# Performance work log

Hardware: AMD Instinct MI355X
Metric: run time of the kernel (lower is better)

## Reference

```python
import jax, jax.numpy as jnp
import numpy as np

B, T, D = 64, 2048, 300

def setup_inputs() -> dict:
    key = jax.random.key(0)
    k1, k2, k3, k4 = jax.random.split(key, 4)
    gate_encoding = jax.random.uniform(k1, (B, T, D), dtype=jnp.float32)
    inputs_encoding = jax.random.normal(k2, (B, T, D), dtype=jnp.float32)
    # kaiming-normal-ish init: std = sqrt(2 / fan_in)
    std = float(np.sqrt(2.0 / D))
    Wz = jax.random.normal(k3, (D, D), dtype=jnp.float32) * std
    Wo = jax.random.normal(k4, (D, D), dtype=jnp.float32) * std
    bz = jnp.zeros((D,), dtype=jnp.float32)
    bo = jnp.zeros((D,), dtype=jnp.float32)
    return {"gate_encoding": gate_encoding, "inputs_encoding": inputs_encoding,
            "Wz": Wz, "bz": bz, "Wo": Wo, "bo": bo}

def reference(gate_encoding, inputs_encoding, Wz, bz, Wo, bo):
    # Batch the two linear projections across all timesteps (torch.nn.Linear: x @ W.T + b)
    z = jnp.tanh(jnp.einsum('btd,ed->bte', inputs_encoding, Wz) + bz)  # [B,T,D]
    o = jnp.tanh(jnp.einsum('btd,ed->bte', inputs_encoding, Wo) + bo)  # [B,T,D]

    # Sequential gated recurrence: c_t = g_t * c_{t-1} + (1 - g_t) * z_t ; h_t = o_t * c_t
    def step(c, gz_o):
        g_t, z_t, o_t = gz_o
        c = g_t * c + (1.0 - g_t) * z_t
        return c, o_t * c

    c0 = jnp.zeros((gate_encoding.shape[0], gate_encoding.shape[2]), dtype=inputs_encoding.dtype)
    # scan over time: move T to leading axis
    _, h = jax.lax.scan(step, c0,
                        (jnp.swapaxes(gate_encoding, 0, 1),
                         jnp.swapaxes(z, 0, 1),
                         jnp.swapaxes(o, 0, 1)))
    return jnp.swapaxes(h, 0, 1)  # [B,T,D]
```

## Files before the change

kernel.cpp:

```cpp
#include <hip/hip_runtime.h>
#include <hip/hip_bf16.h>

typedef _Float16 f16x8 __attribute__((ext_vector_type(8)));
typedef _Float16 f16x4 __attribute__((ext_vector_type(4)));
typedef float f32x4 __attribute__((ext_vector_type(4)));

#define B_SZ 64
#define T_SZ 2048
#define D_SZ 300
#define M_SZ (B_SZ * T_SZ)
#define KP 320
#define NP 640
#define NCHUNK 32
#define CLEN 64

__device__ __forceinline__ void gld_lds16(const void* g, void* l) {
    __builtin_amdgcn_global_load_lds(
        (const __attribute__((address_space(1))) unsigned int*)g,
        (__attribute__((address_space(3))) unsigned int*)l,
        16, 0, 0);
}

__device__ __forceinline__ float fast_tanh(float x) {
    float e = __expf(2.0f * x);
    return 1.0f - 2.0f * __builtin_amdgcn_rcpf(e + 1.0f);
}

__global__ void pack_x(const float* __restrict__ in, _Float16* __restrict__ out) {
    unsigned int i = blockIdx.x * 256u + threadIdx.x;
    f32x4 v = *(const f32x4*)(in + (size_t)i * 4);
#pragma unroll
    for (int j = 0; j < 4; ++j) {
        unsigned int f = i * 4 + j;
        unsigned int row = f / D_SZ;
        unsigned int k = f - row * D_SZ;
        out[(size_t)row * KP + k] = (_Float16)v[j];
    }
}

__global__ void pad_x(_Float16* __restrict__ out) {
    unsigned int i = blockIdx.x * 256u + threadIdx.x;
    unsigned int j = i * 4;
    unsigned int row = j / 20;
    unsigned int k0 = j - row * 20;
    f16x4 z = {};
    *(f16x4*)(out + (size_t)row * KP + 300 + k0) = z;
}

__global__ void pack_w(const float* __restrict__ Wz, const float* __restrict__ Wo,
                       _Float16* __restrict__ W) {
    unsigned int i = blockIdx.x * 256u + threadIdx.x;
    if (i >= NP * KP) return;
    unsigned int n = i / KP;
    unsigned int k = i - n * KP;
    float v = 0.0f;
    if (k < D_SZ) {
        if (n < D_SZ) v = Wz[n * D_SZ + k];
        else if (n >= 320 && n < 320 + D_SZ) v = Wo[(n - 320) * D_SZ + k];
    }
    W[i] = (_Float16)v;
}

__global__ void pack_bias(const float* __restrict__ bz, const float* __restrict__ bo,
                          float* __restrict__ bias) {
    int n = threadIdx.x;
    float v = 0.0f;
    if (n < D_SZ) v = bz[n];
    else if (n >= 320 && n < 320 + D_SZ) v = bo[n - 320];
    bias[n] = v;
}

__global__ __launch_bounds__(256) void gemm_zo(const _Float16* __restrict__ X,
                                               const _Float16* __restrict__ W,
                                               const float* __restrict__ bias,
                                               _Float16* __restrict__ C) {
    __shared__ _Float16 As[3][128 * 32];
    __shared__ _Float16 Bs[3][128 * 32];

    const int tid = threadIdx.x;
    const int lane = tid & 63;
    const int wid = tid >> 6;
    const int wm = wid >> 1, wn = wid & 1;

    int g = blockIdx.x;
    int s = (g & 7) * (5120 / 8) + (g >> 3);
    int bm = s / 5;
    int bn = s - bm * 5;

    f32x4 acc[4][4] = {};

    const int r_in_c = lane >> 2;
    const int u_phys = lane & 3;

    const _Float16* Abase = X + (size_t)(bm * 128) * KP;
    const _Float16* Bbase = W + (size_t)(bn * 128) * KP;

    auto stage = [&](int buf, int kt) {
#pragma unroll
        for (int j = 0; j < 2; ++j) {
            int c = wid + j * 4;
            int row = c * 16 + r_in_c;
            int ul = u_phys ^ ((row >> 1) & 3);
            gld_lds16(Abase + (size_t)row * KP + kt * 32 + ul * 8, &As[buf][c * 512]);
            gld_lds16(Bbase + (size_t)row * KP + kt * 32 + ul * 8, &Bs[buf][c * 512]);
        }
    };

    stage(0, 0);
    stage(1, 1);

#pragma unroll 1
    for (int kt = 0; kt < 10; ++kt) {
        if (kt < 8) {
            stage((kt + 2) % 3, kt + 2);
            asm volatile("s_waitcnt vmcnt(8)" ::: "memory");
        } else if (kt == 8) {
            asm volatile("s_waitcnt vmcnt(4)" ::: "memory");
        } else {
            asm volatile("s_waitcnt vmcnt(0)" ::: "memory");
        }
        __builtin_amdgcn_s_barrier();
        __builtin_amdgcn_sched_barrier(0);

        const int cb = kt % 3;
        f16x8 bf[4], af[4];
#pragma unroll
        for (int ns = 0; ns < 4; ++ns) {
            int row = wn * 64 + ns * 16 + (lane & 15);
            int u = (lane >> 4) ^ ((row >> 1) & 3);
            bf[ns] = *(const f16x8*)&Bs[cb][row * 32 + u * 8];
        }
#pragma unroll
        for (int ms = 0; ms < 4; ++ms) {
            int row = wm * 64 + ms * 16 + (lane & 15);
            int u = (lane >> 4) ^ ((row >> 1) & 3);
            af[ms] = *(const f16x8*)&As[cb][row * 32 + u * 8];
        }
        asm volatile("s_waitcnt lgkmcnt(0)" ::: "memory");
        __builtin_amdgcn_s_barrier();
        __builtin_amdgcn_sched_barrier(0);

        __builtin_amdgcn_s_setprio(1);
#pragma unroll
        for (int ms = 0; ms < 4; ++ms)
#pragma unroll
            for (int ns = 0; ns < 4; ++ns)
                acc[ms][ns] = __builtin_amdgcn_mfma_f32_16x16x32_f16(bf[ns], af[ms], acc[ms][ns], 0, 0, 0);
        __builtin_amdgcn_s_setprio(0);
    }

    const int mrow0 = bm * 128 + wm * 64;
    const int ncol0 = bn * 128 + wn * 64;
#pragma unroll
    for (int ns = 0; ns < 4; ++ns) {
        int nb = ncol0 + ns * 16 + (lane >> 4) * 4;
        f32x4 b4 = *(const f32x4*)&bias[nb];
#pragma unroll
        for (int ms = 0; ms < 4; ++ms) {
            int m = mrow0 + ms * 16 + (lane & 15);
            f16x4 v;
#pragma unroll
            for (int r = 0; r < 4; ++r)
                v[r] = (_Float16)fast_tanh(acc[ms][ns][r] + b4[r]);
            *(f16x4*)&C[(size_t)m * NP + nb] = v;
        }
    }
}

__global__ void scan_p1(const float* __restrict__ gate, const _Float16* __restrict__ C,
                        float* __restrict__ Aout, float* __restrict__ Bout) {
    int b = blockIdx.x >> 5;
    int nc = blockIdx.x & 31;
    int d = threadIdx.x;
    if (d >= D_SZ) return;
    size_t base = (size_t)b * T_SZ + (size_t)nc * CLEN;
    const float* gp = gate + base * D_SZ + d;
    const _Float16* zp = C + base * NP + d;
    float A = 1.0f, Bc = 0.0f;
    for (int t = 0; t < CLEN; ++t) {
        float gv = gp[(size_t)t * D_SZ];
        float zv = (float)zp[(size_t)t * NP];
        A *= gv;
        Bc = gv * Bc + (1.0f - gv) * zv;
    }
    int o = (b * NCHUNK + nc) * D_SZ + d;
    Aout[o] = A;
    Bout[o] = Bc;
}

__global__ void scan_p2(const float* __restrict__ A, const float* __restrict__ Bc,
                        float* __restrict__ Cin) {
    int idx = blockIdx.x * 256 + threadIdx.x;
    if (idx >= B_SZ * D_SZ) return;
    int b = idx / D_SZ;
    int d = idx - b * D_SZ;
    float c = 0.0f;
    for (int nc = 0; nc < NCHUNK; ++nc) {
        int o = (b * NCHUNK + nc) * D_SZ + d;
        Cin[o] = c;
        c = A[o] * c + Bc[o];
    }
}

__global__ void scan_p3(const float* __restrict__ gate, const _Float16* __restrict__ C,
                        const float* __restrict__ Cin, float* __restrict__ out) {
    int b = blockIdx.x >> 5;
    int nc = blockIdx.x & 31;
    int d = threadIdx.x;
    if (d >= D_SZ) return;
    size_t base = (size_t)b * T_SZ + (size_t)nc * CLEN;
    const float* gp = gate + base * D_SZ + d;
    const _Float16* zp = C + base * NP + d;
    const _Float16* op = zp + 320;
    float* hp = out + base * D_SZ + d;
    float c = Cin[(b * NCHUNK + nc) * D_SZ + d];
    for (int t = 0; t < CLEN; ++t) {
        float gv = gp[(size_t)t * D_SZ];
        float zv = (float)zp[(size_t)t * NP];
        float ov = (float)op[(size_t)t * NP];
        c = gv * c + (1.0f - gv) * zv;
        hp[(size_t)t * D_SZ] = ov * c;
    }
}

extern "C" void kernel_launch(void* const* d_in, const int* in_sizes, int n_in,
                              void* d_out, int out_size, void* d_ws, size_t ws_size,
                              hipStream_t stream) {
    const float* gate = (const float*)d_in[0];
    const float* xin  = (const float*)d_in[1];
    const float* Wz   = (const float*)d_in[2];
    const float* bz   = (const float*)d_in[3];
    const float* Wo   = (const float*)d_in[4];
    const float* bo   = (const float*)d_in[5];
    float* out = (float*)d_out;

    char* ws = (char*)d_ws;
    _Float16* Xf16 = (_Float16*)(ws);
    _Float16* C16  = (_Float16*)(ws + 83886080ull);
    _Float16* Wc   = (_Float16*)(ws + 251658240ull);
    float*    bias = (float*)   (ws + 252067840ull);
    float*    Ach  = (float*)   (ws);
    float*    Bch  = (float*)   (ws + 2457600ull);
    float*    Cin  = (float*)   (ws + 4915200ull);

    pack_x<<<(M_SZ * D_SZ / 4) / 256, 256, 0, stream>>>(xin, Xf16);
    pad_x<<<(M_SZ * 20 / 4) / 256, 256, 0, stream>>>(Xf16);
    pack_w<<<(NP * KP + 255) / 256, 256, 0, stream>>>(Wz, Wo, Wc);
    pack_bias<<<1, NP, 0, stream>>>(bz, bo, bias);

    gemm_zo<<<(M_SZ / 128) * (NP / 128), 256, 0, stream>>>(Xf16, Wc, bias, C16);

    scan_p1<<<B_SZ * NCHUNK, 320, 0, stream>>>(gate, C16, Ach, Bch);
    scan_p2<<<(B_SZ * D_SZ + 255) / 256, 256, 0, stream>>>(Ach, Bch, Cin);
    scan_p3<<<B_SZ * NCHUNK, 320, 0, stream>>>(gate, C16, Cin, out);
}
```

Before: 327.4 us.

## Use single-wave 64x64 GEMM tiles, fuse X packing with padding, relocate scan buffers

The GEMM becomes one wavefront per 64x64 output tile with a k-step of 64, double-buffered LDS and no block barriers, in place of a 4-wave 128x128 tile with a three-stage pipeline. The X pack kernel now performs vectorized float4-to-half4 conversion per row and also writes the zero padding, which removes the separate pad kernel. The scan scratch buffers move to workspace offsets that no longer overlap the packed X buffer. Smaller tiles remove barrier synchronisation but reload more operand data per FLOP, and the next-stage load into the same LDS buffers relies on in-order behaviour within a single wave.

```diff
diff --git a/kernel.cpp b/kernel.cpp
--- a/kernel.cpp
+++ b/kernel.cpp
@@ -28,23 +28,18 @@
 
 __global__ void pack_x(const float* __restrict__ in, _Float16* __restrict__ out) {
     unsigned int i = blockIdx.x * 256u + threadIdx.x;
-    f32x4 v = *(const f32x4*)(in + (size_t)i * 4);
-#pragma unroll
-    for (int j = 0; j < 4; ++j) {
-        unsigned int f = i * 4 + j;
-        unsigned int row = f / D_SZ;
-        unsigned int k = f - row * D_SZ;
-        out[(size_t)row * KP + k] = (_Float16)v[j];
-    }
-}
-
-__global__ void pad_x(_Float16* __restrict__ out) {
-    unsigned int i = blockIdx.x * 256u + threadIdx.x;
-    unsigned int j = i * 4;
-    unsigned int row = j / 20;
-    unsigned int k0 = j - row * 20;
-    f16x4 z = {};
-    *(f16x4*)(out + (size_t)row * KP + 300 + k0) = z;
+    unsigned int row = i / 80;
+    unsigned int kq = i - row * 80;
+    if (kq < 75) {
+        f32x4 v = *(const f32x4*)(in + (size_t)row * D_SZ + kq * 4);
+        f16x4 h;
+#pragma unroll
+        for (int r = 0; r < 4; ++r) h[r] = (_Float16)v[r];
+        *(f16x4*)(out + (size_t)row * KP + kq * 4) = h;
+    } else {
+        f16x4 z = {};
+        *(f16x4*)(out + (size_t)row * KP + 300 + (kq - 75) * 4) = z;
+    }
 }
 
 __global__ void pack_w(const float* __restrict__ Wz, const float* __restrict__ Wo,
@@ -70,94 +65,91 @@
     bias[n] = v;
 }
 
-__global__ __launch_bounds__(256) void gemm_zo(const _Float16* __restrict__ X,
-                                               const _Float16* __restrict__ W,
-                                               const float* __restrict__ bias,
-                                               _Float16* __restrict__ C) {
-    __shared__ _Float16 As[3][128 * 32];
-    __shared__ _Float16 Bs[3][128 * 32];
-
-    const int tid = threadIdx.x;
-    const int lane = tid & 63;
-    const int wid = tid >> 6;
-    const int wm = wid >> 1, wn = wid & 1;
-
+__global__ __launch_bounds__(64, 4) void gemm_zo(const _Float16* __restrict__ X,
+                                                 const _Float16* __restrict__ W,
+                                                 const float* __restrict__ bias,
+                                                 _Float16* __restrict__ C) {
+    __shared__ _Float16 As[2][64 * 32];
+    __shared__ _Float16 Bs[2][64 * 32];
+
+    const int lane = threadIdx.x;
     int g = blockIdx.x;
-    int s = (g & 7) * (5120 / 8) + (g >> 3);
-    int bm = s / 5;
-    int bn = s - bm * 5;
-
-    f32x4 acc[4][4] = {};
-
-    const int r_in_c = lane >> 2;
-    const int u_phys = lane & 3;
-
-    const _Float16* Abase = X + (size_t)(bm * 128) * KP;
-    const _Float16* Bbase = W + (size_t)(bn * 128) * KP;
-
-    auto stage = [&](int buf, int kt) {
-#pragma unroll
-        for (int j = 0; j < 2; ++j) {
-            int c = wid + j * 4;
-            int row = c * 16 + r_in_c;
-            int ul = u_phys ^ ((row >> 1) & 3);
-            gld_lds16(Abase + (size_t)row * KP + kt * 32 + ul * 8, &As[buf][c * 512]);
-            gld_lds16(Bbase + (size_t)row * KP + kt * 32 + ul * 8, &Bs[buf][c * 512]);
+    int s = (g & 7) * (20480 / 8) + (g >> 3);
+    int bm = s / 10;
+    int bn = s - bm * 10;
+
+    const int l15 = lane & 15;
+    const int kq = lane >> 4;
+
+    const int r_in = lane >> 2;
+    const int u4 = lane & 3;
+    const int skey = (r_in >> 1) & 3;
+    const int ul = u4 ^ skey;
+
+    const _Float16* Abase = X + (size_t)(bm * 64) * KP;
+    const _Float16* Bbase = W + (size_t)(bn * 64) * KP;
+
+    auto stage = [&](int kt) {
+#pragma unroll
+        for (int ku = 0; ku < 2; ++ku) {
+            int k0 = kt * 64 + ku * 32 + ul * 8;
+#pragma unroll
+            for (int j = 0; j < 4; ++j) {
+                int row = j * 16 + r_in;
+                gld_lds16(Abase + (size_t)row * KP + k0, &As[ku][j * 512]);
+                gld_lds16(Bbase + (size_t)row * KP + k0, &Bs[ku][j * 512]);
+            }
         }
     };
 
-    stage(0, 0);
-    stage(1, 1);
+    f32x4 acc[4][4] = {};
+
+    stage(0);
 
 #pragma unroll 1
-    for (int kt = 0; kt < 10; ++kt) {
-        if (kt < 8) {
-            stage((kt + 2) % 3, kt + 2);
-            asm volatile("s_waitcnt vmcnt(8)" ::: "memory");
-        } else if (kt == 8) {
-            asm volatile("s_waitcnt vmcnt(4)" ::: "memory");
-        } else {
-            asm volatile("s_waitcnt vmcnt(0)" ::: "memory");
+    for (int kt = 0; kt < 5; ++kt) {
+        asm volatile("s_waitcnt vmcnt(0)" ::: "memory");
+        __builtin_amdgcn_sched_barrier(0);
+
+#pragma unroll
+        for (int ku = 0; ku < 2; ++ku) {
+            f16x8 af[4], bf[4];
+#pragma unroll
+            for (int ms = 0; ms < 4; ++ms) {
+                int row = ms * 16 + l15;
+                int u = kq ^ ((row >> 1) & 3);
+                af[ms] = *(const f16x8*)&As[ku][row * 32 + u * 8];
+            }
+#pragma unroll
+            for (int ns = 0; ns < 4; ++ns) {
+                int row = ns * 16 + l15;
+                int u = kq ^ ((row >> 1) & 3);
+                bf[ns] = *(const f16x8*)&Bs[ku][row * 32 + u * 8];
+            }
+            asm volatile("s_waitcnt lgkmcnt(0)" ::: "memory");
+            __builtin_amdgcn_sched_barrier(0);
+
+            if (ku == 1 && kt < 4) stage(kt + 1);
+
+            __builtin_amdgcn_s_setprio(1);
+#pragma unroll
+            for (int ms = 0; ms < 4; ++ms)
+#pragma unroll
+                for (int ns = 0; ns < 4; ++ns)
+                    acc[ms][ns] = __builtin_amdgcn_mfma_f32_16x16x32_f16(bf[ns], af[ms], acc[ms][ns], 0, 0, 0);
+            __builtin_amdgcn_s_setprio(0);
         }
-        __builtin_amdgcn_s_barrier();
-        __builtin_amdgcn_sched_barrier(0);
-
-        const int cb = kt % 3;
-        f16x8 bf[4], af[4];
-#pragma unroll
-        for (int ns = 0; ns < 4; ++ns) {
-            int row = wn * 64 + ns * 16 + (lane & 15);
-            int u = (lane >> 4) ^ ((row >> 1) & 3);
-            bf[ns] = *(const f16x8*)&Bs[cb][row * 32 + u * 8];
-        }
+    }
+
+    const int mrow0 = bm * 64;
+    const int ncol0 = bn * 64;
+#pragma unroll
+    for (int ns = 0; ns < 4; ++ns) {
+        int nb = ncol0 + ns * 16 + kq * 4;
+        f32x4 b4 = *(const f32x4*)&bias[nb];
 #pragma unroll
         for (int ms = 0; ms < 4; ++ms) {
-            int row = wm * 64 + ms * 16 + (lane & 15);
-            int u = (lane >> 4) ^ ((row >> 1) & 3);
-            af[ms] = *(const f16x8*)&As[cb][row * 32 + u * 8];
-        }
-        asm volatile("s_waitcnt lgkmcnt(0)" ::: "memory");
-        __builtin_amdgcn_s_barrier();
-        __builtin_amdgcn_sched_barrier(0);
-
-        __builtin_amdgcn_s_setprio(1);
-#pragma unroll
-        for (int ms = 0; ms < 4; ++ms)
-#pragma unroll
-            for (int ns = 0; ns < 4; ++ns)
-                acc[ms][ns] = __builtin_amdgcn_mfma_f32_16x16x32_f16(bf[ns], af[ms], acc[ms][ns], 0, 0, 0);
-        __builtin_amdgcn_s_setprio(0);
-    }
-
-    const int mrow0 = bm * 128 + wm * 64;
-    const int ncol0 = bn * 128 + wn * 64;
-#pragma unroll
-    for (int ns = 0; ns < 4; ++ns) {
-        int nb = ncol0 + ns * 16 + (lane >> 4) * 4;
-        f32x4 b4 = *(const f32x4*)&bias[nb];
-#pragma unroll
-        for (int ms = 0; ms < 4; ++ms) {
-            int m = mrow0 + ms * 16 + (lane & 15);
+            int m = mrow0 + ms * 16 + l15;
             f16x4 v;
 #pragma unroll
             for (int r = 0; r < 4; ++r)
@@ -239,16 +231,15 @@
     _Float16* C16  = (_Float16*)(ws + 83886080ull);
     _Float16* Wc   = (_Float16*)(ws + 251658240ull);
     float*    bias = (float*)   (ws + 252067840ull);
-    float*    Ach  = (float*)   (ws);
-    float*    Bch  = (float*)   (ws + 2457600ull);
-    float*    Cin  = (float*)   (ws + 4915200ull);
-
-    pack_x<<<(M_SZ * D_SZ / 4) / 256, 256, 0, stream>>>(xin, Xf16);
-    pad_x<<<(M_SZ * 20 / 4) / 256, 256, 0, stream>>>(Xf16);
+    float*    Ach  = (float*)   (ws + 252070400ull);
+    float*    Bch  = (float*)   (ws + 254528000ull);
+    float*    Cin  = (float*)   (ws + 256985600ull);
+
+    pack_x<<<(M_SZ * 80) / 256, 256, 0, stream>>>(xin, Xf16);
     pack_w<<<(NP * KP + 255) / 256, 256, 0, stream>>>(Wz, Wo, Wc);
     pack_bias<<<1, NP, 0, stream>>>(bz, bo, bias);
 
-    gemm_zo<<<(M_SZ / 128) * (NP / 128), 256, 0, stream>>>(Xf16, Wc, bias, C16);
+    gemm_zo<<<(M_SZ / 64) * (NP / 64), 64, 0, stream>>>(Xf16, Wc, bias, C16);
 
     scan_p1<<<B_SZ * NCHUNK, 320, 0, stream>>>(gate, C16, Ach, Bch);
     scan_p2<<<(B_SZ * D_SZ + 255) / 256, 256, 0, stream>>>(Ach, Bch, Cin);
```

Measured after the change: 351.5 us. 1.07x slower.
